# Optimization experiments

Measured on AMD Instinct MI355X. Metric: run time of the kernel, lower is better.

The kernel has to match this reference:

```python
import jax, jax.numpy as jnp
import numpy as np

N_HEAD = 16


def setup_inputs() -> dict:
    key = jax.random.key(0)
    k1, k2, k3 = jax.random.split(key, 3)
    B, T, C = 2, 2048, 1024
    x = jax.random.normal(k1, (B, T, C), dtype=jnp.float32)
    Wqkv = jax.random.normal(k2, (C, 3 * C), dtype=jnp.float32) * 0.02
    bqkv = jnp.zeros((3 * C,), dtype=jnp.float32)
    Wproj = jax.random.normal(k3, (C, C), dtype=jnp.float32) * 0.02
    bproj = jnp.zeros((C,), dtype=jnp.float32)
    return {"x": x, "Wqkv": Wqkv, "bqkv": bqkv, "Wproj": Wproj, "bproj": bproj}


def reference(x, Wqkv, bqkv, Wproj, bproj):
    b, t, c = x.shape
    h = N_HEAD
    d = c // h  # head_dim
    # qkv projection, split into q,k,v per head: (b,t,3,h,d)
    qkv = (x @ Wqkv + bqkv).reshape(b, t, 3, h, d)
    q, k, v = qkv[:, :, 0], qkv[:, :, 1], qkv[:, :, 2]  # each (b,t,h,d)
    # Faithful quirk of original: n_state = head_dim // heads, scale = 1/sqrt(n_state)
    scale = jnp.float32(1.0 / np.sqrt(d // h))
    # attn_mode == 'all': dense non-causal attention
    w = jnp.einsum('bqhd,bkhd->bhqk', q, k)  # (b,h,t,t)
    w = jax.nn.softmax(w * scale, axis=-1)
    a = jnp.einsum('bhqk,bkhd->bqhd', w, v).reshape(b, t, c)
    return a @ Wproj + bproj
```

## Files before the change

kernel.cpp:

```cpp
#include <hip/hip_runtime.h>

typedef float floatx4 __attribute__((ext_vector_type(4)));
typedef __bf16 bf16x8 __attribute__((ext_vector_type(8)));
typedef __bf16 bf16x4 __attribute__((ext_vector_type(4)));

#define MFMA16 __builtin_amdgcn_mfma_f32_16x16x32_bf16

typedef const __attribute__((address_space(1))) void* gas_t;
typedef __attribute__((address_space(3))) void* las_t;
#define GLD16(g, l) __builtin_amdgcn_global_load_lds((gas_t)(g), (las_t)(l), 16, 0, 0)

static __device__ __forceinline__ unsigned short f2bf(float f) {
  union { float f; unsigned int u; } v; v.f = f;
  unsigned int r = v.u + 0x7fffu + ((v.u >> 16) & 1u);
  return (unsigned short)(r >> 16);
}

__global__ void cast_kernel(const float* __restrict__ in,
                            unsigned short* __restrict__ out, int n4) {
  int i = blockIdx.x * blockDim.x + threadIdx.x;
  if (i < n4) {
    float4 v = ((const float4*)in)[i];
    ushort4 o;
    o.x = f2bf(v.x); o.y = f2bf(v.y); o.z = f2bf(v.z); o.w = f2bf(v.w);
    ((ushort4*)out)[i] = o;
  }
}

__global__ __launch_bounds__(256) void cast_transpose(
    const float* __restrict__ in, unsigned short* __restrict__ out,
    int R, int C) {
  const int r0 = blockIdx.y * 64, c0 = blockIdx.x * 64;
  const int tid = threadIdx.x;
  __shared__ float tl[64][65];
  const int rr = tid >> 4, cc = (tid & 15) * 4;
#pragma unroll
  for (int i = 0; i < 4; ++i) {
    int row = rr + i * 16;
    float4 v = *(const float4*)(in + (size_t)(r0 + row) * C + c0 + cc);
    tl[row][cc] = v.x; tl[row][cc + 1] = v.y;
    tl[row][cc + 2] = v.z; tl[row][cc + 3] = v.w;
  }
  __syncthreads();
  const int cl = tid >> 2, rbase = (tid & 3) * 16;
  unsigned short o[16];
#pragma unroll
  for (int j = 0; j < 16; ++j) o[j] = f2bf(tl[rbase + j][cl]);
  unsigned short* dst = out + (size_t)(c0 + cl) * R + r0 + rbase;
  *(uint4*)dst = *(uint4*)o;
  *(uint4*)(dst + 8) = *(uint4*)(o + 8);
}

__global__ __launch_bounds__(256) void gemm_qkv(
    const unsigned short* __restrict__ A,
    const unsigned short* __restrict__ Bt,
    const float* __restrict__ bias,
    unsigned short* __restrict__ Qt,
    unsigned short* __restrict__ Kc,
    unsigned short* __restrict__ Vt) {
  const int K = 1024;
  const int m0 = blockIdx.y * 128, n0 = blockIdx.x * 128;
  const int tid = threadIdx.x, w = tid >> 6, l = tid & 63;
  const int l16 = l & 15, lq = l >> 4;
  const int wm = w >> 1, wn = w & 1;

  __shared__ unsigned short As[128 * 64];
  __shared__ unsigned short Bs[128 * 64];

  floatx4 acc[4][4] = {};

  int sA[4], sB[4];
  unsigned ldso[4];
#pragma unroll
  for (int j = 0; j < 4; ++j) {
    int s = j * 256 + tid;
    int row = s >> 3, blk = (s & 7) ^ (row & 7);
    sA[j] = (m0 + row) * K + blk * 8;
    sB[j] = (n0 + row) * K + blk * 8;
    ldso[j] = (unsigned)(j * 256 + w * 64) * 8;
  }

  for (int k0 = 0; k0 < K; k0 += 64) {
    __syncthreads();
#pragma unroll
    for (int j = 0; j < 4; ++j) {
      GLD16(A + sA[j] + k0, As + ldso[j]);
      GLD16(Bt + sB[j] + k0, Bs + ldso[j]);
    }
    __syncthreads();
#pragma unroll
    for (int kk = 0; kk < 2; ++kk) {
      bf16x8 af[4], bf[4];
#pragma unroll
      for (int mi = 0; mi < 4; ++mi) {
        int row = wm * 64 + mi * 16 + l16;
        int blk = (kk * 4 + lq) ^ (l16 & 7);
        af[mi] = *(const bf16x8*)(As + row * 64 + blk * 8);
      }
#pragma unroll
      for (int ni = 0; ni < 4; ++ni) {
        int row = wn * 64 + ni * 16 + l16;
        int blk = (kk * 4 + lq) ^ (l16 & 7);
        bf[ni] = *(const bf16x8*)(Bs + row * 64 + blk * 8);
      }
#pragma unroll
      for (int ni = 0; ni < 4; ++ni)
#pragma unroll
        for (int mi = 0; mi < 4; ++mi)
          acc[mi][ni] = MFMA16(af[mi], bf[ni], acc[mi][ni], 0, 0, 0);
    }
  }

  const int which = n0 >> 10;
  float bv[4];
#pragma unroll
  for (int ni = 0; ni < 4; ++ni) bv[ni] = bias[n0 + wn * 64 + ni * 16 + l16];
#pragma unroll
  for (int mi = 0; mi < 4; ++mi) {
#pragma unroll
    for (int ni = 0; ni < 4; ++ni) {
      int col = n0 + wn * 64 + ni * 16 + l16;
      int c1 = col & 1023;
      int h = c1 >> 6, dd = c1 & 63;
      int row0 = m0 + wm * 64 + mi * 16 + lq * 4;
      int bb = row0 >> 11, tt0 = row0 & 2047;
      size_t bh = (size_t)(bb * 16 + h);
      if (which == 2) {
        floatx4 vv = acc[mi][ni] + bv[ni];
        *(bf16x4*)(Vt + (bh * 64 + dd) * 2048 + tt0) =
            __builtin_convertvector(vv, bf16x4);
      } else if (which == 0) {
        floatx4 vv = (acc[mi][ni] + bv[ni]) * 0.7213475204444817f;
        *(bf16x4*)(Qt + (bh * 64 + dd) * 2048 + tt0) =
            __builtin_convertvector(vv, bf16x4);
      } else {
#pragma unroll
        for (int r = 0; r < 4; ++r)
          Kc[(bh * 2048 + tt0 + r) * 64 + dd] = f2bf(acc[mi][ni][r] + bv[ni]);
      }
    }
  }
}

__global__ __launch_bounds__(512) void attn_kernel(
    const unsigned short* __restrict__ Qt,
    const unsigned short* __restrict__ Kc,
    const unsigned short* __restrict__ Vt,
    unsigned short* __restrict__ AO) {
  const int T = 2048;
  const int bh = blockIdx.y, q0 = blockIdx.x * 256;
  const int tid = threadIdx.x, w = tid >> 6, l = tid & 63;
  const int l16 = l & 15, lq = l >> 4;

  __shared__ unsigned short Ks[2][64 * 64];
  __shared__ unsigned short Vs[2][64 * 64];
  __shared__ unsigned short Ps[8][32 * 64];

  bf16x8 qf[2][2];
  {
    const unsigned short* qtb = Qt + (size_t)bh * 64 * 2048 + q0 + w * 32;
#pragma unroll
    for (int qs = 0; qs < 2; ++qs) {
      int t = qs * 16 + l16;
#pragma unroll
      for (int c2 = 0; c2 < 2; ++c2)
#pragma unroll
        for (int j = 0; j < 8; ++j) {
          int d = c2 * 32 + lq * 8 + j;
          qf[qs][c2][j] = ((const __bf16*)qtb)[(size_t)d * 2048 + t];
        }
    }
  }

  float l_lane[2] = {0.f, 0.f};
  floatx4 o_acc[4][2] = {};

  const unsigned short* kbase = Kc + (size_t)bh * T * 64;
  const unsigned short* vbase = Vt + (size_t)bh * 64 * T;
  const int srow = tid >> 3, sblk = (tid & 7) ^ (srow & 7);
  const int kro = srow * 64 + sblk * 8;
  const int vro = srow * T + sblk * 8;
  const unsigned ldso = (unsigned)(w * 64) * 8;

  const int swz0 = (0 + lq) ^ (l16 & 7);
  const int swz1 = (4 + lq) ^ (l16 & 7);

  GLD16(kbase + kro, &Ks[0][ldso]);
  GLD16(vbase + vro, &Vs[0][ldso]);

  for (int it = 0; it < 32; ++it) {
    __syncthreads();
    if (it + 1 < 32) {
      int kt = (it + 1) * 64, nb = (it + 1) & 1;
      GLD16(kbase + kt * 64 + kro, &Ks[nb][ldso]);
      GLD16(vbase + kt + vro, &Vs[nb][ldso]);
    }
    const unsigned short* kb = Ks[it & 1];
    const unsigned short* vb = Vs[it & 1];

    floatx4 st[2][4];
#pragma unroll
    for (int ct = 0; ct < 4; ++ct) {
      const unsigned short* kr = kb + (ct * 16 + l16) * 64;
      bf16x8 kf0 = *(const bf16x8*)(kr + swz0 * 8);
      bf16x8 kf1 = *(const bf16x8*)(kr + swz1 * 8);
#pragma unroll
      for (int qs = 0; qs < 2; ++qs) {
        floatx4 z = {};
        z = MFMA16(kf0, qf[qs][0], z, 0, 0, 0);
        z = MFMA16(kf1, qf[qs][1], z, 0, 0, 0);
        st[qs][ct] = z;
      }
    }

    unsigned short* pw = Ps[w];
#pragma unroll
    for (int qs = 0; qs < 2; ++qs) {
#pragma unroll
      for (int ct = 0; ct < 4; ++ct) {
        floatx4 pv;
        pv[0] = __builtin_amdgcn_exp2f(st[qs][ct][0]);
        pv[1] = __builtin_amdgcn_exp2f(st[qs][ct][1]);
        pv[2] = __builtin_amdgcn_exp2f(st[qs][ct][2]);
        pv[3] = __builtin_amdgcn_exp2f(st[qs][ct][3]);
        l_lane[qs] += (pv[0] + pv[1]) + (pv[2] + pv[3]);
        bf16x4 pb = __builtin_convertvector(pv, bf16x4);
        int blk16 = (ct * 2 + (lq >> 1)) ^ (l16 & 7);
        *(bf16x4*)(pw + (qs * 16 + l16) * 64 + blk16 * 8 + (lq & 1) * 4) = pb;
      }
    }

    bf16x8 pf[2][2];
#pragma unroll
    for (int qs = 0; qs < 2; ++qs)
#pragma unroll
      for (int c2 = 0; c2 < 2; ++c2) {
        int blkr = (c2 * 4 + lq) ^ (l16 & 7);
        pf[qs][c2] = *(const bf16x8*)(pw + (qs * 16 + l16) * 64 + blkr * 8);
      }

#pragma unroll
    for (int dt = 0; dt < 4; ++dt) {
      const unsigned short* vr = vb + (dt * 16 + l16) * 64;
      bf16x8 vf0 = *(const bf16x8*)(vr + swz0 * 8);
      bf16x8 vf1 = *(const bf16x8*)(vr + swz1 * 8);
#pragma unroll
      for (int qs = 0; qs < 2; ++qs) {
        o_acc[dt][qs] = MFMA16(vf0, pf[qs][0], o_acc[dt][qs], 0, 0, 0);
        o_acc[dt][qs] = MFMA16(vf1, pf[qs][1], o_acc[dt][qs], 0, 0, 0);
      }
    }
  }

  const int b = bh >> 4, h = bh & 15;
#pragma unroll
  for (int qs = 0; qs < 2; ++qs) {
    float ls = l_lane[qs];
    ls += __shfl_xor(ls, 16, 64);
    ls += __shfl_xor(ls, 32, 64);
    float inv = 1.0f / ls;
    int t = q0 + w * 32 + qs * 16 + l16;
#pragma unroll
    for (int dt = 0; dt < 4; ++dt) {
      floatx4 ov = o_acc[dt][qs] * inv;
      bf16x4 ob = __builtin_convertvector(ov, bf16x4);
      *(bf16x4*)(AO + ((size_t)b * 2048 + t) * 1024 + h * 64 + dt * 16 +
                 lq * 4) = ob;
    }
  }
}

__global__ __launch_bounds__(256) void gemm_proj(
    const unsigned short* __restrict__ A,
    const unsigned short* __restrict__ Bt,
    const float* __restrict__ bias,
    float* __restrict__ out) {
  const int K = 1024, N = 1024;
  const int m0 = blockIdx.y * 128, n0 = blockIdx.x * 64;
  const int tid = threadIdx.x, w = tid >> 6, l = tid & 63;
  const int l16 = l & 15, lq = l >> 4;

  __shared__ unsigned short As[128 * 64];
  __shared__ unsigned short Bs[64 * 64];

  floatx4 acc[2][4] = {};

  int sA[4], sB[2];
  unsigned ldsoA[4], ldsoB[2];
#pragma unroll
  for (int j = 0; j < 4; ++j) {
    int s = j * 256 + tid;
    int row = s >> 3, blk = (s & 7) ^ (row & 7);
    sA[j] = (m0 + row) * K + blk * 8;
    ldsoA[j] = (unsigned)(j * 256 + w * 64) * 8;
  }
#pragma unroll
  for (int j = 0; j < 2; ++j) {
    int s = j * 256 + tid;
    int row = s >> 3, blk = (s & 7) ^ (row & 7);
    sB[j] = (n0 + row) * K + blk * 8;
    ldsoB[j] = (unsigned)(j * 256 + w * 64) * 8;
  }

  for (int k0 = 0; k0 < K; k0 += 64) {
    __syncthreads();
#pragma unroll
    for (int j = 0; j < 4; ++j) GLD16(A + sA[j] + k0, As + ldsoA[j]);
#pragma unroll
    for (int j = 0; j < 2; ++j) GLD16(Bt + sB[j] + k0, Bs + ldsoB[j]);
    __syncthreads();
#pragma unroll
    for (int kk = 0; kk < 2; ++kk) {
      bf16x8 af[2], bf[4];
#pragma unroll
      for (int mi = 0; mi < 2; ++mi) {
        int row = w * 32 + mi * 16 + l16;
        int blk = (kk * 4 + lq) ^ (l16 & 7);
        af[mi] = *(const bf16x8*)(As + row * 64 + blk * 8);
      }
#pragma unroll
      for (int ni = 0; ni < 4; ++ni) {
        int row = ni * 16 + l16;
        int blk = (kk * 4 + lq) ^ (l16 & 7);
        bf[ni] = *(const bf16x8*)(Bs + row * 64 + blk * 8);
      }
#pragma unroll
      for (int ni = 0; ni < 4; ++ni)
#pragma unroll
        for (int mi = 0; mi < 2; ++mi)
          acc[mi][ni] = MFMA16(af[mi], bf[ni], acc[mi][ni], 0, 0, 0);
    }
  }

#pragma unroll
  for (int ni = 0; ni < 4; ++ni) {
    int col = n0 + ni * 16 + l16;
    float bv = bias[col];
#pragma unroll
    for (int mi = 0; mi < 2; ++mi) {
#pragma unroll
      for (int r = 0; r < 4; ++r) {
        int row = m0 + w * 32 + mi * 16 + lq * 4 + r;
        out[(size_t)row * N + col] = acc[mi][ni][r] + bv;
      }
    }
  }
}

extern "C" void kernel_launch(void* const* d_in, const int* in_sizes, int n_in,
                              void* d_out, int out_size, void* d_ws,
                              size_t ws_size, hipStream_t stream) {
  const float* x     = (const float*)d_in[0];
  const float* Wqkv  = (const float*)d_in[1];
  const float* bqkv  = (const float*)d_in[2];
  const float* Wproj = (const float*)d_in[3];
  const float* bproj = (const float*)d_in[4];
  float* out = (float*)d_out;

  unsigned short* Xb     = (unsigned short*)d_ws;
  unsigned short* Wqkvt  = Xb + 4194304;
  unsigned short* Wprojt = Wqkvt + 3145728;
  unsigned short* Qtb    = Wprojt + 1048576;
  unsigned short* Kb     = Qtb + 4194304;
  unsigned short* Vtb    = Kb + 4194304;
  unsigned short* AOb    = Vtb + 4194304;

  cast_kernel<<<4096, 256, 0, stream>>>(x, Xb, 1048576);
  cast_transpose<<<dim3(48, 16), 256, 0, stream>>>(Wqkv, Wqkvt, 1024, 3072);
  cast_transpose<<<dim3(16, 16), 256, 0, stream>>>(Wproj, Wprojt, 1024, 1024);

  gemm_qkv<<<dim3(24, 32), 256, 0, stream>>>(Xb, Wqkvt, bqkv, Qtb, Kb, Vtb);
  attn_kernel<<<dim3(8, 32), 512, 0, stream>>>(Qtb, Kb, Vtb, AOb);
  gemm_proj<<<dim3(16, 32), 256, 0, stream>>>(AOb, Wprojt, bproj, out);
}
```

Baseline: 199.5 us.

## Vectorize K and output stores via swapped MFMA operands; shrink attention blocks

In the QKV GEMM, K-tiles now swap the MFMA operand order so each lane holds four contiguous head-dim values. The strided scalar K stores become 8-byte vector stores. The projection GEMM uses the same trick to write float4 rows instead of scalar strided floats. The attention kernel moves from 256-query/512-thread blocks to 128-query/256-thread blocks, doubling the grid and halving LDS per block. This should raise occupancy and improve load balance across CUs, but each K/V tile is now loaded by twice as many blocks.

New measurement: 209.3 us. 4.9% more time.

```diff
diff --git a/kernel.cpp b/kernel.cpp
--- a/kernel.cpp
+++ b/kernel.cpp
@@ -63,6 +63,7 @@
   const int tid = threadIdx.x, w = tid >> 6, l = tid & 63;
   const int l16 = l & 15, lq = l >> 4;
   const int wm = w >> 1, wn = w & 1;
+  const int which = n0 >> 10;
 
   __shared__ unsigned short As[128 * 64];
   __shared__ unsigned short Bs[128 * 64];
@@ -80,81 +81,123 @@
     ldso[j] = (unsigned)(j * 256 + w * 64) * 8;
   }
 
-  for (int k0 = 0; k0 < K; k0 += 64) {
-    __syncthreads();
-#pragma unroll
-    for (int j = 0; j < 4; ++j) {
-      GLD16(A + sA[j] + k0, As + ldso[j]);
-      GLD16(Bt + sB[j] + k0, Bs + ldso[j]);
-    }
-    __syncthreads();
-#pragma unroll
-    for (int kk = 0; kk < 2; ++kk) {
-      bf16x8 af[4], bf[4];
-#pragma unroll
-      for (int mi = 0; mi < 4; ++mi) {
-        int row = wm * 64 + mi * 16 + l16;
-        int blk = (kk * 4 + lq) ^ (l16 & 7);
-        af[mi] = *(const bf16x8*)(As + row * 64 + blk * 8);
-      }
+  if (which != 1) {
+    for (int k0 = 0; k0 < K; k0 += 64) {
+      __syncthreads();
+#pragma unroll
+      for (int j = 0; j < 4; ++j) {
+        GLD16(A + sA[j] + k0, As + ldso[j]);
+        GLD16(Bt + sB[j] + k0, Bs + ldso[j]);
+      }
+      __syncthreads();
+#pragma unroll
+      for (int kk = 0; kk < 2; ++kk) {
+        bf16x8 af[4], bf[4];
+#pragma unroll
+        for (int mi = 0; mi < 4; ++mi) {
+          int row = wm * 64 + mi * 16 + l16;
+          int blk = (kk * 4 + lq) ^ (l16 & 7);
+          af[mi] = *(const bf16x8*)(As + row * 64 + blk * 8);
+        }
+#pragma unroll
+        for (int ni = 0; ni < 4; ++ni) {
+          int row = wn * 64 + ni * 16 + l16;
+          int blk = (kk * 4 + lq) ^ (l16 & 7);
+          bf[ni] = *(const bf16x8*)(Bs + row * 64 + blk * 8);
+        }
+#pragma unroll
+        for (int ni = 0; ni < 4; ++ni)
+#pragma unroll
+          for (int mi = 0; mi < 4; ++mi)
+            acc[mi][ni] = MFMA16(af[mi], bf[ni], acc[mi][ni], 0, 0, 0);
+      }
+    }
+    float bv[4];
+#pragma unroll
+    for (int ni = 0; ni < 4; ++ni) bv[ni] = bias[n0 + wn * 64 + ni * 16 + l16];
+#pragma unroll
+    for (int mi = 0; mi < 4; ++mi) {
 #pragma unroll
       for (int ni = 0; ni < 4; ++ni) {
-        int row = wn * 64 + ni * 16 + l16;
-        int blk = (kk * 4 + lq) ^ (l16 & 7);
-        bf[ni] = *(const bf16x8*)(Bs + row * 64 + blk * 8);
-      }
-#pragma unroll
-      for (int ni = 0; ni < 4; ++ni)
-#pragma unroll
-        for (int mi = 0; mi < 4; ++mi)
-          acc[mi][ni] = MFMA16(af[mi], bf[ni], acc[mi][ni], 0, 0, 0);
-    }
-  }
-
-  const int which = n0 >> 10;
-  float bv[4];
-#pragma unroll
-  for (int ni = 0; ni < 4; ++ni) bv[ni] = bias[n0 + wn * 64 + ni * 16 + l16];
-#pragma unroll
-  for (int mi = 0; mi < 4; ++mi) {
-#pragma unroll
-    for (int ni = 0; ni < 4; ++ni) {
-      int col = n0 + wn * 64 + ni * 16 + l16;
-      int c1 = col & 1023;
-      int h = c1 >> 6, dd = c1 & 63;
-      int row0 = m0 + wm * 64 + mi * 16 + lq * 4;
-      int bb = row0 >> 11, tt0 = row0 & 2047;
-      size_t bh = (size_t)(bb * 16 + h);
-      if (which == 2) {
-        floatx4 vv = acc[mi][ni] + bv[ni];
-        *(bf16x4*)(Vt + (bh * 64 + dd) * 2048 + tt0) =
+        int col = n0 + wn * 64 + ni * 16 + l16;
+        int c1 = col & 1023;
+        int h = c1 >> 6, dd = c1 & 63;
+        int row0 = m0 + wm * 64 + mi * 16 + lq * 4;
+        int bb = row0 >> 11, tt0 = row0 & 2047;
+        size_t bh = (size_t)(bb * 16 + h);
+        if (which == 2) {
+          floatx4 vv = acc[mi][ni] + bv[ni];
+          *(bf16x4*)(Vt + (bh * 64 + dd) * 2048 + tt0) =
+              __builtin_convertvector(vv, bf16x4);
+        } else {
+          floatx4 vv = (acc[mi][ni] + bv[ni]) * 0.7213475204444817f;
+          *(bf16x4*)(Qt + (bh * 64 + dd) * 2048 + tt0) =
+              __builtin_convertvector(vv, bf16x4);
+        }
+      }
+    }
+  } else {
+    for (int k0 = 0; k0 < K; k0 += 64) {
+      __syncthreads();
+#pragma unroll
+      for (int j = 0; j < 4; ++j) {
+        GLD16(A + sA[j] + k0, As + ldso[j]);
+        GLD16(Bt + sB[j] + k0, Bs + ldso[j]);
+      }
+      __syncthreads();
+#pragma unroll
+      for (int kk = 0; kk < 2; ++kk) {
+        bf16x8 af[4], bf[4];
+#pragma unroll
+        for (int mi = 0; mi < 4; ++mi) {
+          int row = wm * 64 + mi * 16 + l16;
+          int blk = (kk * 4 + lq) ^ (l16 & 7);
+          af[mi] = *(const bf16x8*)(As + row * 64 + blk * 8);
+        }
+#pragma unroll
+        for (int ni = 0; ni < 4; ++ni) {
+          int row = wn * 64 + ni * 16 + l16;
+          int blk = (kk * 4 + lq) ^ (l16 & 7);
+          bf[ni] = *(const bf16x8*)(Bs + row * 64 + blk * 8);
+        }
+#pragma unroll
+        for (int ni = 0; ni < 4; ++ni)
+#pragma unroll
+          for (int mi = 0; mi < 4; ++mi)
+            acc[mi][ni] = MFMA16(bf[ni], af[mi], acc[mi][ni], 0, 0, 0);
+      }
+    }
+#pragma unroll
+    for (int mi = 0; mi < 4; ++mi) {
+      int t_g = m0 + wm * 64 + mi * 16 + l16;
+      int bb = t_g >> 11, tt = t_g & 2047;
+#pragma unroll
+      for (int ni = 0; ni < 4; ++ni) {
+        int col0 = n0 + wn * 64 + ni * 16 + lq * 4;
+        floatx4 bv = *(const floatx4*)(bias + col0);
+        floatx4 vv = acc[mi][ni] + bv;
+        int h = (col0 & 1023) >> 6, dd0 = col0 & 63;
+        size_t bh = (size_t)(bb * 16 + h);
+        *(bf16x4*)(Kc + (bh * 2048 + tt) * 64 + dd0) =
             __builtin_convertvector(vv, bf16x4);
-      } else if (which == 0) {
-        floatx4 vv = (acc[mi][ni] + bv[ni]) * 0.7213475204444817f;
-        *(bf16x4*)(Qt + (bh * 64 + dd) * 2048 + tt0) =
-            __builtin_convertvector(vv, bf16x4);
-      } else {
-#pragma unroll
-        for (int r = 0; r < 4; ++r)
-          Kc[(bh * 2048 + tt0 + r) * 64 + dd] = f2bf(acc[mi][ni][r] + bv[ni]);
-      }
-    }
-  }
-}
-
-__global__ __launch_bounds__(512) void attn_kernel(
+      }
+    }
+  }
+}
+
+__global__ __launch_bounds__(256) void attn_kernel(
     const unsigned short* __restrict__ Qt,
     const unsigned short* __restrict__ Kc,
     const unsigned short* __restrict__ Vt,
     unsigned short* __restrict__ AO) {
   const int T = 2048;
-  const int bh = blockIdx.y, q0 = blockIdx.x * 256;
+  const int bh = blockIdx.y, q0 = blockIdx.x * 128;
   const int tid = threadIdx.x, w = tid >> 6, l = tid & 63;
   const int l16 = l & 15, lq = l >> 4;
 
   __shared__ unsigned short Ks[2][64 * 64];
   __shared__ unsigned short Vs[2][64 * 64];
-  __shared__ unsigned short Ps[8][32 * 64];
+  __shared__ unsigned short Ps[4][32 * 64];
 
   bf16x8 qf[2][2];
   {
@@ -177,23 +220,35 @@
 
   const unsigned short* kbase = Kc + (size_t)bh * T * 64;
   const unsigned short* vbase = Vt + (size_t)bh * 64 * T;
-  const int srow = tid >> 3, sblk = (tid & 7) ^ (srow & 7);
-  const int kro = srow * 64 + sblk * 8;
-  const int vro = srow * T + sblk * 8;
-  const unsigned ldso = (unsigned)(w * 64) * 8;
+  int kro[2], vro[2];
+  unsigned ldso[2];
+#pragma unroll
+  for (int j = 0; j < 2; ++j) {
+    int s = j * 256 + tid;
+    int row = s >> 3, blk = (s & 7) ^ (row & 7);
+    kro[j] = row * 64 + blk * 8;
+    vro[j] = row * T + blk * 8;
+    ldso[j] = (unsigned)(j * 256 + w * 64) * 8;
+  }
 
   const int swz0 = (0 + lq) ^ (l16 & 7);
   const int swz1 = (4 + lq) ^ (l16 & 7);
 
-  GLD16(kbase + kro, &Ks[0][ldso]);
-  GLD16(vbase + vro, &Vs[0][ldso]);
+#pragma unroll
+  for (int j = 0; j < 2; ++j) {
+    GLD16(kbase + kro[j], &Ks[0][ldso[j]]);
+    GLD16(vbase + vro[j], &Vs[0][ldso[j]]);
+  }
 
   for (int it = 0; it < 32; ++it) {
     __syncthreads();
     if (it + 1 < 32) {
       int kt = (it + 1) * 64, nb = (it + 1) & 1;
-      GLD16(kbase + kt * 64 + kro, &Ks[nb][ldso]);
-      GLD16(vbase + kt + vro, &Vs[nb][ldso]);
+#pragma unroll
+      for (int j = 0; j < 2; ++j) {
+        GLD16(kbase + kt * 64 + kro[j], &Ks[nb][ldso[j]]);
+        GLD16(vbase + kt + vro[j], &Vs[nb][ldso[j]]);
+      }
     }
     const unsigned short* kb = Ks[it & 1];
     const unsigned short* vb = Vs[it & 1];
@@ -328,21 +383,18 @@
       for (int ni = 0; ni < 4; ++ni)
 #pragma unroll
         for (int mi = 0; mi < 2; ++mi)
-          acc[mi][ni] = MFMA16(af[mi], bf[ni], acc[mi][ni], 0, 0, 0);
-    }
-  }
-
-#pragma unroll
-  for (int ni = 0; ni < 4; ++ni) {
-    int col = n0 + ni * 16 + l16;
-    float bv = bias[col];
-#pragma unroll
-    for (int mi = 0; mi < 2; ++mi) {
-#pragma unroll
-      for (int r = 0; r < 4; ++r) {
-        int row = m0 + w * 32 + mi * 16 + lq * 4 + r;
-        out[(size_t)row * N + col] = acc[mi][ni][r] + bv;
-      }
+          acc[mi][ni] = MFMA16(bf[ni], af[mi], acc[mi][ni], 0, 0, 0);
+    }
+  }
+
+#pragma unroll
+  for (int mi = 0; mi < 2; ++mi) {
+    int t = m0 + w * 32 + mi * 16 + l16;
+#pragma unroll
+    for (int ni = 0; ni < 4; ++ni) {
+      int col0 = n0 + ni * 16 + lq * 4;
+      floatx4 bv = *(const floatx4*)(bias + col0);
+      *(floatx4*)(out + (size_t)t * N + col0) = acc[mi][ni] + bv;
     }
   }
 }
@@ -370,6 +422,6 @@
   cast_transpose<<<dim3(16, 16), 256, 0, stream>>>(Wproj, Wprojt, 1024, 1024);
 
   gemm_qkv<<<dim3(24, 32), 256, 0, stream>>>(Xb, Wqkvt, bqkv, Qtb, Kb, Vtb);
-  attn_kernel<<<dim3(8, 32), 512, 0, stream>>>(Qtb, Kb, Vtb, AOb);
+  attn_kernel<<<dim3(16, 32), 256, 0, stream>>>(Qtb, Kb, Vtb, AOb);
   gemm_proj<<<dim3(16, 32), 256, 0, stream>>>(AOb, Wprojt, bproj, out);
 }
```
